# Kernel tuning notes

Hardware: AMD Instinct MI355X
Metric: run time of the kernel (lower is better)

Reference implementation:

```python
import jax, jax.numpy as jnp
import numpy as np
from jax.ops import segment_sum

N_NODES = 100000
N_EDGES = 1600000
HIDDEN = 64
N_LAYERS = 4
N_CLASSES = 10
N_GRAPHS = 512


def setup_inputs() -> dict:
    key = jax.random.key(0)
    ks = jax.random.split(key, 9)
    x = jax.random.normal(ks[0], (N_NODES, HIDDEN), dtype=jnp.float32)
    edge_index = jax.random.randint(ks[1], (2, N_EDGES), 0, N_NODES, dtype=jnp.int32)
    batch = jnp.sort(jax.random.randint(ks[2], (N_NODES,), 0, N_GRAPHS, dtype=jnp.int32))
    s = 0.05
    W_enc = jax.random.normal(ks[3], (HIDDEN, HIDDEN), dtype=jnp.float32) * s
    b_enc = jax.random.normal(ks[4], (HIDDEN,), dtype=jnp.float32) * s
    W_conv = jax.random.normal(ks[5], (N_LAYERS, HIDDEN, HIDDEN), dtype=jnp.float32) * s
    b_conv = jax.random.normal(ks[6], (N_LAYERS, HIDDEN), dtype=jnp.float32) * s
    W_out = jax.random.normal(ks[7], (HIDDEN, N_CLASSES), dtype=jnp.float32) * s
    b_out = jax.random.normal(ks[8], (N_CLASSES,), dtype=jnp.float32) * s
    return {"x": x, "edge_index": edge_index, "batch": batch,
            "W_enc": W_enc, "b_enc": b_enc, "W_conv": W_conv, "b_conv": b_conv,
            "W_out": W_out, "b_out": b_out, "num_graphs": N_GRAPHS}


def reference(x, edge_index, batch, W_enc, b_enc, W_conv, b_conv, W_out, b_out, num_graphs):
    N = x.shape[0]
    src, dst = edge_index[0], edge_index[1]
    # atom_encoder: Linear
    h = x @ W_enc + b_enc
    # GCN symmetric normalization with self-loops (PyG GCNConv default):
    # deg counts incoming edges (dst) plus the self-loop.
    deg = segment_sum(jnp.ones_like(src, dtype=h.dtype), dst, num_segments=N) + 1.0
    deg_inv_sqrt = jax.lax.rsqrt(deg)
    deg_inv = 1.0 / deg  # self-loop norm = d^-1/2 * d^-1/2
    edge_norm = (deg_inv_sqrt[src] * deg_inv_sqrt[dst])[:, None]  # [E,1]
    for l in range(W_conv.shape[0]):
        hl = h @ W_conv[l]                          # [N,H]
        msg = hl[src] * edge_norm                   # gather + normalize [E,H]
        agg = segment_sum(msg, dst, num_segments=N) # scatter-add
        h = agg + hl * deg_inv[:, None] + b_conv[l] # self-loop + bias
        h = jax.nn.silu(h)                          # dropout p=0 / eval: identity
    # global_add_pool over graph ids
    pooled = segment_sum(h, batch, num_segments=num_graphs)  # [G,H]
    # readout: Linear + ReLU (make_mlp with hidden_layers=1)
    out = jax.nn.relu(pooled @ W_out + b_out)
    return out
```

## Files before the change

kernel.cpp:

```cpp
#include <hip/hip_runtime.h>
#include <math.h>

#define HIDDEN 64
#define N_LAYERS 4
#define N_CLASSES 10
#define N_GRAPHS 512
#define BSH 8
#define NPB 256
#define PART_K 2048

typedef _Float16 __h;
typedef __attribute__((ext_vector_type(4))) _Float16 half4;
typedef __attribute__((ext_vector_type(8))) _Float16 half8;
typedef __attribute__((ext_vector_type(4))) float f32x4;

__global__ __launch_bounds__(256) void k_histA(const int* __restrict__ dst,
                                               int* __restrict__ ghist, int E, int NB) {
    __shared__ int hist[512];
    int t = threadIdx.x;
    hist[t] = 0; hist[t + 256] = 0;
    __syncthreads();
    int base = blockIdx.x * PART_K;
    int kend = min(PART_K, E - base);
    for (int k = t; k < kend; k += 256) atomicAdd(&hist[dst[base + k] >> BSH], 1);
    __syncthreads();
    for (int j = t; j < NB; j += 256) {
        int h = hist[j];
        if (h) atomicAdd(&ghist[j], h);
    }
}

__global__ __launch_bounds__(256) void k_bucketscan(const int* __restrict__ ghist,
                                                    int* __restrict__ bucketbase,
                                                    int* __restrict__ gcur, int NB) {
    __shared__ int s[256];
    int t = threadIdx.x;
    int j0 = 2 * t, j1 = 2 * t + 1;
    int h0 = (j0 < NB) ? ghist[j0] : 0;
    int h1 = (j1 < NB) ? ghist[j1] : 0;
    s[t] = h0 + h1; __syncthreads();
    for (int o = 1; o < 256; o <<= 1) {
        int x = (t >= o) ? s[t - o] : 0;
        __syncthreads();
        s[t] += x;
        __syncthreads();
    }
    int base = (t == 0) ? 0 : s[t - 1];
    if (j0 <= NB) { bucketbase[j0] = base;      gcur[j0] = base; }
    if (j1 <= NB) { bucketbase[j1] = base + h0; gcur[j1] = base + h0; }
}

__global__ __launch_bounds__(256) void k_partition(const int* __restrict__ src,
                                                   const int* __restrict__ dst,
                                                   int* __restrict__ gcur,
                                                   int* __restrict__ packed,
                                                   int E, int NB) {
    __shared__ int hist[512];
    __shared__ int scanE[512];
    __shared__ int cur[512];
    __shared__ int delta[512];
    __shared__ int ps[256];
    __shared__ int stage[PART_K];
    int t = threadIdx.x;
    int base = blockIdx.x * PART_K;
    int kend = min(PART_K, E - base);

    hist[t] = 0; hist[t + 256] = 0;
    __syncthreads();
    for (int k = t; k < kend; k += 256) atomicAdd(&hist[dst[base + k] >> BSH], 1);
    __syncthreads();

    int j0 = 2 * t, j1 = j0 + 1;
    int h0 = hist[j0], h1 = hist[j1];
    ps[t] = h0 + h1; __syncthreads();
    for (int o = 1; o < 256; o <<= 1) {
        int x = (t >= o) ? ps[t - o] : 0;
        __syncthreads();
        ps[t] += x;
        __syncthreads();
    }
    int bexc = (t == 0) ? 0 : ps[t - 1];
    scanE[j0] = bexc;
    scanE[j1] = bexc + h0;
    __syncthreads();

    for (int j = t; j < NB; j += 256) {
        int h = hist[j];
        int g = h ? atomicAdd(&gcur[j], h) : 0;
        delta[j] = g - scanE[j];
        cur[j]   = scanE[j];
    }
    __syncthreads();

    for (int k = t; k < kend; k += 256) {
        int d = dst[base + k], s = src[base + k];
        int j = d >> BSH;
        int pos = atomicAdd(&cur[j], 1);
        stage[pos] = (s << BSH) | (d & (NPB - 1));
    }
    __syncthreads();

    for (int i = t; i < kend; i += 256) {
        int lo = 0, hi = NB;
        while (hi - lo > 1) {
            int mid = (lo + hi) >> 1;
            if (scanE[mid] <= i) lo = mid; else hi = mid;
        }
        packed[i + delta[lo]] = stage[i];
    }
}

__global__ __launch_bounds__(256) void k_fill3(const int* __restrict__ packed,
                                               const int* __restrict__ bucketbase,
                                               int* __restrict__ rowptr,
                                               float* __restrict__ dis,
                                               int* __restrict__ csr_src,
                                               int N, int E) {
    __shared__ int cnt[256];
    __shared__ int rp[256];
    int j = blockIdx.x;
    int t = threadIdx.x;
    int node0 = j << BSH;
    int segb = bucketbase[j];
    int sege = bucketbase[j + 1];

    cnt[t] = 0; __syncthreads();
    for (int i = segb + t; i < sege; i += 256) atomicAdd(&cnt[packed[i] & (NPB - 1)], 1);
    __syncthreads();

    int c = cnt[t];
    rp[t] = c; __syncthreads();
    for (int o = 1; o < 256; o <<= 1) {
        int x = (t >= o) ? rp[t - o] : 0;
        __syncthreads();
        rp[t] += x;
        __syncthreads();
    }
    int node = node0 + t;
    int start = segb + rp[t] - c + node;
    if (node < N) {
        rowptr[node] = start;
        dis[node] = rsqrtf((float)c + 1.0f);
        csr_src[start] = node;
        if (node == N - 1) rowptr[N] = E + N;
    }
    __syncthreads();
    cnt[t] = start + 1;
    __syncthreads();
    for (int i = segb + t; i < sege; i += 256) {
        int v = packed[i];
        int slot = atomicAdd(&cnt[v & (NPB - 1)], 1);
        csr_src[slot] = v >> BSH;
    }
}

__device__ __forceinline__ half4 shfl_xor_h4(half4 v, int m) {
    uint2 u = __builtin_bit_cast(uint2, v);
    u.x = __shfl_xor((int)u.x, m);
    u.y = __shfl_xor((int)u.y, m);
    return __builtin_bit_cast(half4, u);
}

__global__ __launch_bounds__(256) void k_prepW(const float* __restrict__ Wconv,
                                               const float* __restrict__ Wenc,
                                               __h* __restrict__ Wh) {
    int idx = blockIdx.x * 256 + threadIdx.x;
    int l = idx >> 12;
    int kn = idx & 4095;
    int k = kn >> 6, n = kn & 63;
    int nt = n >> 4, nl = n & 15;
    int kt = k >> 5, kr = k & 31;
    int quad = kr >> 3, j = kr & 7;
    int lane = quad * 16 + nl;
    int pos = (((nt * 2 + kt) * 64 + lane) << 3) + j;
    float w = (l < N_LAYERS) ? Wconv[(size_t)l * 4096 + kn] : Wenc[kn];
    Wh[(l << 12) + pos] = (__h)w;
}

__global__ __launch_bounds__(256) void k_gather(const int* __restrict__ csr_src,
                                                const int* __restrict__ rowptr,
                                                const float* __restrict__ dis,
                                                const __h* __restrict__ G,
                                                __h* __restrict__ AGG, int N) {
    int node = blockIdx.x * 4 + (threadIdx.x >> 6);
    if (node >= N) return;
    int lane = threadIdx.x & 63;
    int grp  = lane >> 4;
    int f4   = lane & 15;
    int beg  = rowptr[node];
    int end  = rowptr[node + 1];

    const half4 z = {(__h)0.f, (__h)0.f, (__h)0.f, (__h)0.f};
    half4 a = z;
    int e = beg + grp;
    while (e < end) {
        int s0 = csr_src[e];
        int s1 = (e + 4  < end) ? csr_src[e + 4]  : -1;
        int s2 = (e + 8  < end) ? csr_src[e + 8]  : -1;
        int s3 = (e + 12 < end) ? csr_src[e + 12] : -1;
        int s4 = (e + 16 < end) ? csr_src[e + 16] : -1;
        int s5 = (e + 20 < end) ? csr_src[e + 20] : -1;
        int s6 = (e + 24 < end) ? csr_src[e + 24] : -1;
        int s7 = (e + 28 < end) ? csr_src[e + 28] : -1;
        half4 r0 = ((const half4*)(G + (size_t)s0 * 64))[f4];
        half4 r1 = (s1 >= 0) ? ((const half4*)(G + (size_t)s1 * 64))[f4] : z;
        half4 r2 = (s2 >= 0) ? ((const half4*)(G + (size_t)s2 * 64))[f4] : z;
        half4 r3 = (s3 >= 0) ? ((const half4*)(G + (size_t)s3 * 64))[f4] : z;
        half4 r4 = (s4 >= 0) ? ((const half4*)(G + (size_t)s4 * 64))[f4] : z;
        half4 r5 = (s5 >= 0) ? ((const half4*)(G + (size_t)s5 * 64))[f4] : z;
        half4 r6 = (s6 >= 0) ? ((const half4*)(G + (size_t)s6 * 64))[f4] : z;
        half4 r7 = (s7 >= 0) ? ((const half4*)(G + (size_t)s7 * 64))[f4] : z;
        a += r0; a += r1; a += r2; a += r3;
        a += r4; a += r5; a += r6; a += r7;
        e += 32;
    }
    a += shfl_xor_h4(a, 16);
    a += shfl_xor_h4(a, 32);

    if (grp == 0) {
        __h dd = (__h)dis[node];
        half4 o = a * dd;
        ((half4*)(AGG + (size_t)node * 64))[f4] = o;
    }
}

__global__ __launch_bounds__(256) void k_gemm_mfma(const __h* __restrict__ in,
                                                   const float* __restrict__ xf,
                                                   const __h* __restrict__ Wh,
                                                   const float* __restrict__ bias,
                                                   const float* __restrict__ dis,
                                                   const int* __restrict__ batch,
                                                   __h* __restrict__ Gho,
                                                   float* __restrict__ pooled,
                                                   int N, int mode) {
    int wave = threadIdx.x >> 6;
    int lane = threadIdx.x & 63;
    int row0 = (blockIdx.x * 4 + wave) * 32;
    if (row0 >= N) return;
    int quad = lane >> 4, nl = lane & 15;

    half8 bf[4][2];
    #pragma unroll
    for (int nt = 0; nt < 4; ++nt)
        #pragma unroll
        for (int kt = 0; kt < 2; ++kt)
            bf[nt][kt] = *(const half8*)(Wh + (((nt * 2 + kt) * 64 + lane) << 3));

    f32x4 acc[2][4];
    #pragma unroll
    for (int h = 0; h < 2; ++h) {
        int r = row0 + h * 16 + nl; if (r >= N) r = N - 1;
        half8 a0, a1;
        if (mode == 0) {
            const float* ap = xf + (size_t)r * 64 + quad * 8;
            float4 v0 = ((const float4*)ap)[0];
            float4 v1 = ((const float4*)ap)[1];
            float4 v2 = ((const float4*)(ap + 32))[0];
            float4 v3 = ((const float4*)(ap + 32))[1];
            a0 = (half8){(__h)v0.x, (__h)v0.y, (__h)v0.z, (__h)v0.w,
                         (__h)v1.x, (__h)v1.y, (__h)v1.z, (__h)v1.w};
            a1 = (half8){(__h)v2.x, (__h)v2.y, (__h)v2.z, (__h)v2.w,
                         (__h)v3.x, (__h)v3.y, (__h)v3.z, (__h)v3.w};
        } else {
            const __h* ap = in + (size_t)r * 64 + quad * 8;
            a0 = *(const half8*)(ap);
            a1 = *(const half8*)(ap + 32);
        }
        #pragma unroll
        for (int nt = 0; nt < 4; ++nt) {
            acc[h][nt] = (f32x4){0.f, 0.f, 0.f, 0.f};
            acc[h][nt] = __builtin_amdgcn_mfma_f32_16x16x32_f16(a0, bf[nt][0], acc[h][nt], 0, 0, 0);
            acc[h][nt] = __builtin_amdgcn_mfma_f32_16x16x32_f16(a1, bf[nt][1], acc[h][nt], 0, 0, 0);
        }
    }

    float b[4];
    #pragma unroll
    for (int nt = 0; nt < 4; ++nt) b[nt] = bias[nt * 16 + nl];

    if (mode != 2) {
        #pragma unroll
        for (int h = 0; h < 2; ++h) {
            #pragma unroll
            for (int reg = 0; reg < 4; ++reg) {
                int rr = row0 + h * 16 + quad * 4 + reg;
                if (rr < N) {
                    float ds = dis[rr];
                    #pragma unroll
                    for (int nt = 0; nt < 4; ++nt) {
                        float v = acc[h][nt][reg] + b[nt];
                        if (mode == 1) v = v / (1.0f + expf(-v));
                        Gho[(size_t)rr * 64 + nt * 16 + nl] = (__h)(ds * v);
                    }
                }
            }
        }
    } else {
        float run[4] = {0.f, 0.f, 0.f, 0.f};
        int cur = -1;
        #pragma unroll
        for (int h = 0; h < 2; ++h) {
            #pragma unroll
            for (int reg = 0; reg < 4; ++reg) {
                int rr = row0 + h * 16 + quad * 4 + reg;
                if (rr < N) {
                    int bi = batch[rr];
                    float vals[4];
                    #pragma unroll
                    for (int nt = 0; nt < 4; ++nt) {
                        float v = acc[h][nt][reg] + b[nt];
                        vals[nt] = v / (1.0f + expf(-v));
                    }
                    if (bi != cur) {
                        if (cur >= 0) {
                            #pragma unroll
                            for (int nt = 0; nt < 4; ++nt)
                                atomicAdd(&pooled[cur * 64 + nt * 16 + nl], run[nt]);
                        }
                        cur = bi;
                        #pragma unroll
                        for (int nt = 0; nt < 4; ++nt) run[nt] = vals[nt];
                    } else {
                        #pragma unroll
                        for (int nt = 0; nt < 4; ++nt) run[nt] += vals[nt];
                    }
                }
            }
        }
        if (cur >= 0) {
            #pragma unroll
            for (int nt = 0; nt < 4; ++nt)
                atomicAdd(&pooled[cur * 64 + nt * 16 + nl], run[nt]);
        }
    }
}

__global__ __launch_bounds__(256) void k_readout(const float* __restrict__ pooled,
                                                 const float* __restrict__ Wout,
                                                 const float* __restrict__ bout,
                                                 float* __restrict__ out) {
    int idx = blockIdx.x * 256 + threadIdx.x;
    if (idx >= N_GRAPHS * N_CLASSES) return;
    int g = idx / N_CLASSES, c = idx % N_CLASSES;
    float s = bout[c];
    #pragma unroll
    for (int j = 0; j < 64; ++j) s += pooled[g * 64 + j] * Wout[j * N_CLASSES + c];
    out[idx] = fmaxf(s, 0.0f);
}

extern "C" void kernel_launch(void* const* d_in, const int* in_sizes, int n_in,
                              void* d_out, int out_size, void* d_ws, size_t ws_size,
                              hipStream_t stream) {
    const float* x      = (const float*)d_in[0];
    const int*   ei     = (const int*)d_in[1];
    const int*   batch  = (const int*)d_in[2];
    const float* W_enc  = (const float*)d_in[3];
    const float* b_enc  = (const float*)d_in[4];
    const float* W_conv = (const float*)d_in[5];
    const float* b_conv = (const float*)d_in[6];
    const float* W_out  = (const float*)d_in[7];
    const float* b_out  = (const float*)d_in[8];
    float* out = (float*)d_out;

    const int N = in_sizes[2];
    const int E = in_sizes[1] / 2;
    const int* src = ei;
    const int* dst = ei + E;
    const int NB   = (N + NPB - 1) >> BSH;
    const int NBLK = (E + PART_K - 1) / PART_K;

    char* ws = (char*)d_ws;
    size_t off = 0;
    auto alloc = [&](size_t bytes) -> char* {
        char* p = ws + off;
        off += (bytes + 255) & ~(size_t)255;
        return p;
    };
    int*   ghist      = (int*)alloc((size_t)(NB + 1) * sizeof(int));
    int*   bucketbase = (int*)alloc((size_t)(NB + 1) * sizeof(int));
    int*   gcur       = (int*)alloc((size_t)(NB + 1) * sizeof(int));
    int*   packed     = (int*)alloc((size_t)E * sizeof(int));
    int*   csr_src    = (int*)alloc((size_t)(E + N) * sizeof(int));
    int*   rowptr     = (int*)alloc((size_t)(N + 1) * sizeof(int));
    float* dis        = (float*)alloc((size_t)N * sizeof(float));
    __h*   GhA        = (__h*)alloc((size_t)N * HIDDEN * sizeof(__h));
    __h*   AGGh       = (__h*)alloc((size_t)N * HIDDEN * sizeof(__h));
    __h*   Wh         = (__h*)alloc((size_t)(N_LAYERS + 1) * 4096 * sizeof(__h));
    float* pooled     = (float*)alloc((size_t)N_GRAPHS * HIDDEN * sizeof(float));
    (void)ws_size;

    hipMemsetAsync(ghist, 0, (size_t)(NB + 1) * sizeof(int), stream);
    hipMemsetAsync(pooled, 0, (size_t)N_GRAPHS * HIDDEN * sizeof(float), stream);

    k_histA     <<<NBLK, 256, 0, stream>>>(dst, ghist, E, NB);
    k_bucketscan<<<1,    256, 0, stream>>>(ghist, bucketbase, gcur, NB);
    k_partition <<<NBLK, 256, 0, stream>>>(src, dst, gcur, packed, E, NB);
    k_fill3     <<<NB,   256, 0, stream>>>(packed, bucketbase, rowptr, dis, csr_src, N, E);
    k_prepW<<<((N_LAYERS + 1) * 4096) / 256, 256, 0, stream>>>(W_conv, W_enc, Wh);

    int gb32 = (N + 127) / 128;
    k_gemm_mfma<<<gb32, 256, 0, stream>>>(nullptr, x, Wh + (size_t)N_LAYERS * 4096, b_enc,
                                          dis, batch, GhA, pooled, N, 0);

    for (int l = 0; l < N_LAYERS; ++l) {
        int last = (l == N_LAYERS - 1);
        k_gather<<<(N + 3) / 4, 256, 0, stream>>>(csr_src, rowptr, dis, GhA, AGGh, N);
        k_gemm_mfma<<<gb32, 256, 0, stream>>>(AGGh, nullptr, Wh + (size_t)l * 4096,
                                              b_conv + (size_t)l * HIDDEN, dis, batch,
                                              GhA, pooled, N, last ? 2 : 1);
    }

    k_readout<<<(N_GRAPHS * N_CLASSES + 255) / 256, 256, 0, stream>>>(pooled, W_out, b_out, out);
}
```

Before: 386.9 us.

## Fuse per-layer gather with MFMA GEMM and drop partition binary search

Merges the neighbor-aggregation kernel and the per-layer MFMA GEMM into one kernel. Each wave aggregates 16 nodes into shared memory, then runs the 16x64x64 MFMA, SiLU and pooling epilogue itself, with ping-pong output buffers. This removes the intermediate AGG write/read round-trip and one launch per layer. In the partition kernel, the per-element binary search for the bucket is replaced by a stored 16-bit bucket id per staged edge. The cost is that each wave now processes 16 nodes serially during the gather phase, which reduces memory-level parallelism per node.

```diff
diff --git a/kernel.cpp b/kernel.cpp
--- a/kernel.cpp
+++ b/kernel.cpp
@@ -61,6 +61,7 @@
     __shared__ int delta[512];
     __shared__ int ps[256];
     __shared__ int stage[PART_K];
+    __shared__ unsigned short stgj[PART_K];
     int t = threadIdx.x;
     int base = blockIdx.x * PART_K;
     int kend = min(PART_K, E - base);
@@ -97,16 +98,12 @@
         int j = d >> BSH;
         int pos = atomicAdd(&cur[j], 1);
         stage[pos] = (s << BSH) | (d & (NPB - 1));
+        stgj[pos]  = (unsigned short)j;
     }
     __syncthreads();
 
     for (int i = t; i < kend; i += 256) {
-        int lo = 0, hi = NB;
-        while (hi - lo > 1) {
-            int mid = (lo + hi) >> 1;
-            if (scanE[mid] <= i) lo = mid; else hi = mid;
-        }
-        packed[i + delta[lo]] = stage[i];
+        packed[i + delta[stgj[i]]] = stage[i];
     }
 }
 
@@ -177,62 +174,144 @@
     Wh[(l << 12) + pos] = (__h)w;
 }
 
-__global__ __launch_bounds__(256) void k_gather(const int* __restrict__ csr_src,
-                                                const int* __restrict__ rowptr,
-                                                const float* __restrict__ dis,
-                                                const __h* __restrict__ G,
-                                                __h* __restrict__ AGG, int N) {
-    int node = blockIdx.x * 4 + (threadIdx.x >> 6);
-    if (node >= N) return;
+__global__ __launch_bounds__(256) void k_layer(const int* __restrict__ csr_src,
+                                               const int* __restrict__ rowptr,
+                                               const float* __restrict__ dis,
+                                               const __h* __restrict__ G,
+                                               const __h* __restrict__ Wh,
+                                               const float* __restrict__ bias,
+                                               const int* __restrict__ batch,
+                                               __h* __restrict__ Gho,
+                                               float* __restrict__ pooled,
+                                               int N, int last) {
+    __shared__ __attribute__((aligned(16))) __h At[4][16][72];
+    int wave = threadIdx.x >> 6;
     int lane = threadIdx.x & 63;
-    int grp  = lane >> 4;
-    int f4   = lane & 15;
-    int beg  = rowptr[node];
-    int end  = rowptr[node + 1];
+    int row0 = (blockIdx.x * 4 + wave) * 16;
+    if (row0 >= N) return;
+    int grp = lane >> 4;
+    int f4  = lane & 15;
+
+    int rpi = row0 + lane;
+    int rpv = rowptr[rpi > N ? N : rpi];
 
     const half4 z = {(__h)0.f, (__h)0.f, (__h)0.f, (__h)0.f};
-    half4 a = z;
-    int e = beg + grp;
-    while (e < end) {
-        int s0 = csr_src[e];
-        int s1 = (e + 4  < end) ? csr_src[e + 4]  : -1;
-        int s2 = (e + 8  < end) ? csr_src[e + 8]  : -1;
-        int s3 = (e + 12 < end) ? csr_src[e + 12] : -1;
-        int s4 = (e + 16 < end) ? csr_src[e + 16] : -1;
-        int s5 = (e + 20 < end) ? csr_src[e + 20] : -1;
-        int s6 = (e + 24 < end) ? csr_src[e + 24] : -1;
-        int s7 = (e + 28 < end) ? csr_src[e + 28] : -1;
-        half4 r0 = ((const half4*)(G + (size_t)s0 * 64))[f4];
-        half4 r1 = (s1 >= 0) ? ((const half4*)(G + (size_t)s1 * 64))[f4] : z;
-        half4 r2 = (s2 >= 0) ? ((const half4*)(G + (size_t)s2 * 64))[f4] : z;
-        half4 r3 = (s3 >= 0) ? ((const half4*)(G + (size_t)s3 * 64))[f4] : z;
-        half4 r4 = (s4 >= 0) ? ((const half4*)(G + (size_t)s4 * 64))[f4] : z;
-        half4 r5 = (s5 >= 0) ? ((const half4*)(G + (size_t)s5 * 64))[f4] : z;
-        half4 r6 = (s6 >= 0) ? ((const half4*)(G + (size_t)s6 * 64))[f4] : z;
-        half4 r7 = (s7 >= 0) ? ((const half4*)(G + (size_t)s7 * 64))[f4] : z;
-        a += r0; a += r1; a += r2; a += r3;
-        a += r4; a += r5; a += r6; a += r7;
-        e += 32;
-    }
-    a += shfl_xor_h4(a, 16);
-    a += shfl_xor_h4(a, 32);
-
-    if (grp == 0) {
-        __h dd = (__h)dis[node];
-        half4 o = a * dd;
-        ((half4*)(AGG + (size_t)node * 64))[f4] = o;
-    }
-}
-
-__global__ __launch_bounds__(256) void k_gemm_mfma(const __h* __restrict__ in,
-                                                   const float* __restrict__ xf,
+    for (int i = 0; i < 16; ++i) {
+        int beg = __shfl(rpv, i);
+        int end = __shfl(rpv, i + 1);
+        half4 a = z;
+        int e = beg + grp;
+        while (e < end) {
+            int s0 = csr_src[e];
+            int s1 = (e + 4  < end) ? csr_src[e + 4]  : -1;
+            int s2 = (e + 8  < end) ? csr_src[e + 8]  : -1;
+            int s3 = (e + 12 < end) ? csr_src[e + 12] : -1;
+            int s4 = (e + 16 < end) ? csr_src[e + 16] : -1;
+            int s5 = (e + 20 < end) ? csr_src[e + 20] : -1;
+            int s6 = (e + 24 < end) ? csr_src[e + 24] : -1;
+            int s7 = (e + 28 < end) ? csr_src[e + 28] : -1;
+            half4 r0 = ((const half4*)(G + (size_t)s0 * 64))[f4];
+            half4 r1 = (s1 >= 0) ? ((const half4*)(G + (size_t)s1 * 64))[f4] : z;
+            half4 r2 = (s2 >= 0) ? ((const half4*)(G + (size_t)s2 * 64))[f4] : z;
+            half4 r3 = (s3 >= 0) ? ((const half4*)(G + (size_t)s3 * 64))[f4] : z;
+            half4 r4 = (s4 >= 0) ? ((const half4*)(G + (size_t)s4 * 64))[f4] : z;
+            half4 r5 = (s5 >= 0) ? ((const half4*)(G + (size_t)s5 * 64))[f4] : z;
+            half4 r6 = (s6 >= 0) ? ((const half4*)(G + (size_t)s6 * 64))[f4] : z;
+            half4 r7 = (s7 >= 0) ? ((const half4*)(G + (size_t)s7 * 64))[f4] : z;
+            a += r0; a += r1; a += r2; a += r3;
+            a += r4; a += r5; a += r6; a += r7;
+            e += 32;
+        }
+        a += shfl_xor_h4(a, 16);
+        a += shfl_xor_h4(a, 32);
+        if (grp == 0) {
+            int node = row0 + i;
+            float df = (node < N) ? dis[node] : 0.0f;
+            __h dd = (__h)df;
+            ((half4*)&At[wave][i][0])[f4] = a * dd;
+        }
+    }
+
+    int quad = grp, nl = f4;
+    half8 bf[4][2];
+    #pragma unroll
+    for (int nt = 0; nt < 4; ++nt)
+        #pragma unroll
+        for (int kt = 0; kt < 2; ++kt)
+            bf[nt][kt] = *(const half8*)(Wh + (((nt * 2 + kt) * 64 + lane) << 3));
+
+    half8 a0 = *(const half8*)&At[wave][nl][quad * 8];
+    half8 a1 = *(const half8*)&At[wave][nl][32 + quad * 8];
+
+    f32x4 acc[4];
+    #pragma unroll
+    for (int nt = 0; nt < 4; ++nt) {
+        acc[nt] = (f32x4){0.f, 0.f, 0.f, 0.f};
+        acc[nt] = __builtin_amdgcn_mfma_f32_16x16x32_f16(a0, bf[nt][0], acc[nt], 0, 0, 0);
+        acc[nt] = __builtin_amdgcn_mfma_f32_16x16x32_f16(a1, bf[nt][1], acc[nt], 0, 0, 0);
+    }
+
+    float b[4];
+    #pragma unroll
+    for (int nt = 0; nt < 4; ++nt) b[nt] = bias[nt * 16 + nl];
+
+    if (!last) {
+        #pragma unroll
+        for (int reg = 0; reg < 4; ++reg) {
+            int rr = row0 + quad * 4 + reg;
+            if (rr < N) {
+                float ds_ = dis[rr];
+                #pragma unroll
+                for (int nt = 0; nt < 4; ++nt) {
+                    float v = acc[nt][reg] + b[nt];
+                    v = v / (1.0f + expf(-v));
+                    Gho[(size_t)rr * 64 + nt * 16 + nl] = (__h)(ds_ * v);
+                }
+            }
+        }
+    } else {
+        float run[4] = {0.f, 0.f, 0.f, 0.f};
+        int cur = -1;
+        #pragma unroll
+        for (int reg = 0; reg < 4; ++reg) {
+            int rr = row0 + quad * 4 + reg;
+            if (rr < N) {
+                int bi = batch[rr];
+                float vals[4];
+                #pragma unroll
+                for (int nt = 0; nt < 4; ++nt) {
+                    float v = acc[nt][reg] + b[nt];
+                    vals[nt] = v / (1.0f + expf(-v));
+                }
+                if (bi != cur) {
+                    if (cur >= 0) {
+                        #pragma unroll
+                        for (int nt = 0; nt < 4; ++nt)
+                            atomicAdd(&pooled[cur * 64 + nt * 16 + nl], run[nt]);
+                    }
+                    cur = bi;
+                    #pragma unroll
+                    for (int nt = 0; nt < 4; ++nt) run[nt] = vals[nt];
+                } else {
+                    #pragma unroll
+                    for (int nt = 0; nt < 4; ++nt) run[nt] += vals[nt];
+                }
+            }
+        }
+        if (cur >= 0) {
+            #pragma unroll
+            for (int nt = 0; nt < 4; ++nt)
+                atomicAdd(&pooled[cur * 64 + nt * 16 + nl], run[nt]);
+        }
+    }
+}
+
+__global__ __launch_bounds__(256) void k_gemm_mfma(const float* __restrict__ xf,
                                                    const __h* __restrict__ Wh,
                                                    const float* __restrict__ bias,
                                                    const float* __restrict__ dis,
-                                                   const int* __restrict__ batch,
                                                    __h* __restrict__ Gho,
-                                                   float* __restrict__ pooled,
-                                                   int N, int mode) {
+                                                   int N) {
     int wave = threadIdx.x >> 6;
     int lane = threadIdx.x & 63;
     int row0 = (blockIdx.x * 4 + wave) * 32;
@@ -250,22 +329,15 @@
     #pragma unroll
     for (int h = 0; h < 2; ++h) {
         int r = row0 + h * 16 + nl; if (r >= N) r = N - 1;
-        half8 a0, a1;
-        if (mode == 0) {
-            const float* ap = xf + (size_t)r * 64 + quad * 8;
-            float4 v0 = ((const float4*)ap)[0];
-            float4 v1 = ((const float4*)ap)[1];
-            float4 v2 = ((const float4*)(ap + 32))[0];
-            float4 v3 = ((const float4*)(ap + 32))[1];
-            a0 = (half8){(__h)v0.x, (__h)v0.y, (__h)v0.z, (__h)v0.w,
-                         (__h)v1.x, (__h)v1.y, (__h)v1.z, (__h)v1.w};
-            a1 = (half8){(__h)v2.x, (__h)v2.y, (__h)v2.z, (__h)v2.w,
-                         (__h)v3.x, (__h)v3.y, (__h)v3.z, (__h)v3.w};
-        } else {
-            const __h* ap = in + (size_t)r * 64 + quad * 8;
-            a0 = *(const half8*)(ap);
-            a1 = *(const half8*)(ap + 32);
-        }
+        const float* ap = xf + (size_t)r * 64 + quad * 8;
+        float4 v0 = ((const float4*)ap)[0];
+        float4 v1 = ((const float4*)ap)[1];
+        float4 v2 = ((const float4*)(ap + 32))[0];
+        float4 v3 = ((const float4*)(ap + 32))[1];
+        half8 a0 = (half8){(__h)v0.x, (__h)v0.y, (__h)v0.z, (__h)v0.w,
+                           (__h)v1.x, (__h)v1.y, (__h)v1.z, (__h)v1.w};
+        half8 a1 = (half8){(__h)v2.x, (__h)v2.y, (__h)v2.z, (__h)v2.w,
+                           (__h)v3.x, (__h)v3.y, (__h)v3.z, (__h)v3.w};
         #pragma unroll
         for (int nt = 0; nt < 4; ++nt) {
             acc[h][nt] = (f32x4){0.f, 0.f, 0.f, 0.f};
@@ -278,59 +350,19 @@
     #pragma unroll
     for (int nt = 0; nt < 4; ++nt) b[nt] = bias[nt * 16 + nl];
 
-    if (mode != 2) {
-        #pragma unroll
-        for (int h = 0; h < 2; ++h) {
-            #pragma unroll
-            for (int reg = 0; reg < 4; ++reg) {
-                int rr = row0 + h * 16 + quad * 4 + reg;
-                if (rr < N) {
-                    float ds = dis[rr];
-                    #pragma unroll
-                    for (int nt = 0; nt < 4; ++nt) {
-                        float v = acc[h][nt][reg] + b[nt];
-                        if (mode == 1) v = v / (1.0f + expf(-v));
-                        Gho[(size_t)rr * 64 + nt * 16 + nl] = (__h)(ds * v);
-                    }
+    #pragma unroll
+    for (int h = 0; h < 2; ++h) {
+        #pragma unroll
+        for (int reg = 0; reg < 4; ++reg) {
+            int rr = row0 + h * 16 + quad * 4 + reg;
+            if (rr < N) {
+                float ds = dis[rr];
+                #pragma unroll
+                for (int nt = 0; nt < 4; ++nt) {
+                    float v = acc[h][nt][reg] + b[nt];
+                    Gho[(size_t)rr * 64 + nt * 16 + nl] = (__h)(ds * v);
                 }
             }
-        }
-    } else {
-        float run[4] = {0.f, 0.f, 0.f, 0.f};
-        int cur = -1;
-        #pragma unroll
-        for (int h = 0; h < 2; ++h) {
-            #pragma unroll
-            for (int reg = 0; reg < 4; ++reg) {
-                int rr = row0 + h * 16 + quad * 4 + reg;
-                if (rr < N) {
-                    int bi = batch[rr];
-                    float vals[4];
-                    #pragma unroll
-                    for (int nt = 0; nt < 4; ++nt) {
-                        float v = acc[h][nt][reg] + b[nt];
-                        vals[nt] = v / (1.0f + expf(-v));
-                    }
-                    if (bi != cur) {
-                        if (cur >= 0) {
-                            #pragma unroll
-                            for (int nt = 0; nt < 4; ++nt)
-                                atomicAdd(&pooled[cur * 64 + nt * 16 + nl], run[nt]);
-                        }
-                        cur = bi;
-                        #pragma unroll
-                        for (int nt = 0; nt < 4; ++nt) run[nt] = vals[nt];
-                    } else {
-                        #pragma unroll
-                        for (int nt = 0; nt < 4; ++nt) run[nt] += vals[nt];
-                    }
-                }
-            }
-        }
-        if (cur >= 0) {
-            #pragma unroll
-            for (int nt = 0; nt < 4; ++nt)
-                atomicAdd(&pooled[cur * 64 + nt * 16 + nl], run[nt]);
         }
     }
 }
@@ -383,8 +415,8 @@
     int*   csr_src    = (int*)alloc((size_t)(E + N) * sizeof(int));
     int*   rowptr     = (int*)alloc((size_t)(N + 1) * sizeof(int));
     float* dis        = (float*)alloc((size_t)N * sizeof(float));
-    __h*   GhA        = (__h*)alloc((size_t)N * HIDDEN * sizeof(__h));
-    __h*   AGGh       = (__h*)alloc((size_t)N * HIDDEN * sizeof(__h));
+    __h*   bufA       = (__h*)alloc((size_t)N * HIDDEN * sizeof(__h));
+    __h*   bufB       = (__h*)alloc((size_t)N * HIDDEN * sizeof(__h));
     __h*   Wh         = (__h*)alloc((size_t)(N_LAYERS + 1) * 4096 * sizeof(__h));
     float* pooled     = (float*)alloc((size_t)N_GRAPHS * HIDDEN * sizeof(float));
     (void)ws_size;
@@ -399,15 +431,17 @@
     k_prepW<<<((N_LAYERS + 1) * 4096) / 256, 256, 0, stream>>>(W_conv, W_enc, Wh);
 
     int gb32 = (N + 127) / 128;
-    k_gemm_mfma<<<gb32, 256, 0, stream>>>(nullptr, x, Wh + (size_t)N_LAYERS * 4096, b_enc,
-                                          dis, batch, GhA, pooled, N, 0);
-
+    k_gemm_mfma<<<gb32, 256, 0, stream>>>(x, Wh + (size_t)N_LAYERS * 4096, b_enc,
+                                          dis, bufA, N);
+
+    __h* bufs[2] = {bufA, bufB};
+    int glayer = (N + 63) / 64;
     for (int l = 0; l < N_LAYERS; ++l) {
         int last = (l == N_LAYERS - 1);
-        k_gather<<<(N + 3) / 4, 256, 0, stream>>>(csr_src, rowptr, dis, GhA, AGGh, N);
-        k_gemm_mfma<<<gb32, 256, 0, stream>>>(AGGh, nullptr, Wh + (size_t)l * 4096,
-                                              b_conv + (size_t)l * HIDDEN, dis, batch,
-                                              GhA, pooled, N, last ? 2 : 1);
+        k_layer<<<glayer, 256, 0, stream>>>(csr_src, rowptr, dis, bufs[l & 1],
+                                            Wh + (size_t)l * 4096,
+                                            b_conv + (size_t)l * HIDDEN, batch,
+                                            bufs[(l + 1) & 1], pooled, N, last);
     }
 
     k_readout<<<(N_GRAPHS * N_CLASSES + 255) / 256, 256, 0, stream>>>(pooled, W_out, b_out, out);
```

Result: faster. 336.8 us (-12.9%).
